# Performance work log

Measured on AMD Instinct MI355X. Metric: run time of the kernel, lower is better.

Reference implementation:

```python
import jax, jax.numpy as jnp
import numpy as np

VOCAB, HID, EMB, KSZ, VSZ = 34, 512, 128, 128, 128
T, N, L = 1024, 128, 200


def setup_inputs() -> dict:
    key = jax.random.key(0)
    ks = jax.random.split(key, 20)
    s = 0.05
    emb = jax.random.normal(ks[0], (VOCAB, EMB), jnp.float32) * s
    emb = emb.at[0].set(0.0)  # padding_idx=0
    inp = {
        "key_proj": jax.random.normal(ks[1], (T, N, KSZ), jnp.float32),
        "values": jax.random.normal(ks[2], (T, N, VSZ), jnp.float32),
        "reduced_length": jax.random.randint(ks[3], (N,), 1, T + 1),
        "text": jax.random.randint(ks[4], (N, L), 1, VOCAB),
        "embedding": emb,
        "Wq": jax.random.normal(ks[5], (KSZ, EMB), jnp.float32) * s,
        "bq": jnp.zeros((KSZ,), jnp.float32),
        "W_ih1": jax.random.normal(ks[6], (4 * HID, EMB + VSZ), jnp.float32) * s,
        "W_hh1": jax.random.normal(ks[7], (4 * HID, HID), jnp.float32) * s,
        "b_ih1": jnp.zeros((4 * HID,), jnp.float32),
        "b_hh1": jnp.zeros((4 * HID,), jnp.float32),
        "W_ih2": jax.random.normal(ks[8], (4 * KSZ, HID), jnp.float32) * s,
        "W_hh2": jax.random.normal(ks[9], (4 * KSZ, KSZ), jnp.float32) * s,
        "b_ih2": jnp.zeros((4 * KSZ,), jnp.float32),
        "b_hh2": jnp.zeros((4 * KSZ,), jnp.float32),
        "Wfc": jax.random.normal(ks[10], (EMB, KSZ * 2), jnp.float32) * s,
        "bfc": jnp.zeros((EMB,), jnp.float32),
        "b_out": jnp.zeros((VOCAB,), jnp.float32),
    }
    return inp


def _lstm_cell(x, h, c, Wih, Whh, bih, bhh):
    g = x @ Wih.T + bih + h @ Whh.T + bhh
    i, f, gg, o = jnp.split(g, 4, axis=1)
    c = jax.nn.sigmoid(f) * c + jax.nn.sigmoid(i) * jnp.tanh(gg)
    h = jax.nn.sigmoid(o) * jnp.tanh(c)
    return h, c


def reference(key_proj, values, reduced_length, text, embedding, Wq, bq,
              W_ih1, W_hh1, b_ih1, b_hh1, W_ih2, W_hh2, b_ih2, b_hh2,
              Wfc, bfc, b_out):
    n, l = text.shape
    keyT = jnp.transpose(key_proj, (1, 0, 2))   # (N,T,K)
    valT = jnp.transpose(values, (1, 0, 2))     # (N,T,V)
    t_len = keyT.shape[1]
    mask = jnp.arange(t_len)[None, :] >= reduced_length[:, None]  # (N,T) True=pad

    def attend(q):  # q: (N,K)
        energy = jnp.einsum('ntk,nk->nt', keyT, q)
        energy = jnp.where(mask, -1e9, energy)
        att = jax.nn.softmax(energy, axis=1)
        ctx = jnp.einsum('nt,ntv->nv', att, valT)
        return ctx

    # deterministic teacher forcing: step 0 uses embedding[0] (padding row),
    # step i uses embedding of text[:, i-1]
    char_seq = jnp.concatenate(
        [jnp.broadcast_to(embedding[0], (n, 1, embedding.shape[1])),
         embedding[text[:, :-1]]], axis=1)          # (N,L,E)
    char_seq = jnp.transpose(char_seq, (1, 0, 2))   # (L,N,E)

    h1 = jnp.zeros((n, W_hh1.shape[1]), jnp.float32)
    c1 = jnp.zeros_like(h1)
    h2 = jnp.zeros((n, W_hh2.shape[1]), jnp.float32)
    c2 = jnp.zeros_like(h2)

    def step(carry, ce):
        h1, c1, h2, c2 = carry
        q1 = ce @ Wq.T + bq
        ctx1 = attend(q1)
        inp = jnp.concatenate([ce, ctx1], axis=1)
        h1, c1 = _lstm_cell(inp, h1, c1, W_ih1, W_hh1, b_ih1, b_hh1)
        h2, c2 = _lstm_cell(h1, h2, c2, W_ih2, W_hh2, b_ih2, b_hh2)
        q2 = h2 @ Wq.T + bq
        ctx2 = attend(q2)
        out = jnp.concatenate([h2, ctx2], axis=1) @ Wfc.T + bfc
        out = jnp.clip(out, -1.0, 1.0)  # Hardtanh
        pred = out @ embedding.T + b_out  # tied output weights
        return (h1, c1, h2, c2), pred

    _, preds = jax.lax.scan(step, (h1, c1, h2, c2), char_seq)  # (L,N,V)
    return jnp.transpose(preds, (1, 0, 2))  # (N,L,V)
```

## Files before the change

kernel.cpp:

```cpp
#include <hip/hip_runtime.h>
#include <hip/hip_bf16.h>
#include <math.h>

#define T_LEN 1024
#define NB    128
#define L_SEQ 200
#define EMB   128
#define KSZ   128
#define VSZ   128
#define HID   512
#define G1    2048
#define G2    512
#define VOCAB 34
#define KK1   768
#define KK2   640
#define LB    10

typedef __attribute__((ext_vector_type(8))) short bf16x8;
typedef __attribute__((ext_vector_type(4))) float f32x4;

__device__ __forceinline__ float sig_(float x) { return 1.0f / (1.0f + __expf(-x)); }

__device__ __forceinline__ f32x4 MFMA_BF16(bf16x8 a, bf16x8 b, f32x4 c) {
    return __builtin_amdgcn_mfma_f32_16x16x32_bf16(a, b, c, 0, 0, 0);
}
__device__ __forceinline__ bf16x8 LD8(const __hip_bfloat16* p) {
    return *(const bf16x8*)p;
}

__global__ __launch_bounds__(256) void prep_kernel(
    const float* __restrict__ Wih1, const float* __restrict__ Whh1,
    const float* __restrict__ bih1, const float* __restrict__ bhh1,
    const float* __restrict__ Wih2, const float* __restrict__ Whh2,
    const float* __restrict__ bih2, const float* __restrict__ bhh2,
    __hip_bfloat16* __restrict__ Wc1, __hip_bfloat16* __restrict__ Wc2,
    float* __restrict__ bb1, float* __restrict__ bb2,
    __hip_bfloat16* __restrict__ h1b, __hip_bfloat16* __restrict__ h2b,
    float* __restrict__ c1, float* __restrict__ c2)
{
    const int gid = blockIdx.x * 256 + threadIdx.x;
    if (gid < G1 * KK1) {
        const int o = gid / KK1, k = gid - o * KK1;
        const float v = (k < 256) ? Wih1[o * 256 + k] : Whh1[o * 512 + (k - 256)];
        Wc1[gid] = __float2bfloat16(v);
    }
    if (gid < G2 * KK2) {
        const int o = gid / KK2, k = gid - o * KK2;
        const float v = (k < 512) ? Wih2[o * 512 + k] : Whh2[o * 128 + (k - 512)];
        Wc2[gid] = __float2bfloat16(v);
    }
    if (gid < G1) bb1[gid] = bih1[gid] + bhh1[gid];
    if (gid < G2) bb2[gid] = bih2[gid] + bhh2[gid];
    if (gid < 2 * NB * HID) h1b[gid] = __float2bfloat16(0.0f);
    if (gid < 2 * NB * KSZ) h2b[gid] = __float2bfloat16(0.0f);
    if (gid < NB * HID) c1[gid] = 0.0f;
    if (gid < NB * KSZ) c2[gid] = 0.0f;
}

__global__ __launch_bounds__(256) void transpose_key(
    const float* __restrict__ key, float* __restrict__ keyT2)
{
    __shared__ float tl[32][129];
    const int n = blockIdx.x >> 5;
    const int t0 = (blockIdx.x & 31) << 5;
    for (int idx = threadIdx.x; idx < 32 * 128; idx += 256) {
        const int ti = idx >> 7, k = idx & 127;
        tl[ti][k] = key[((size_t)(t0 + ti) * NB + n) * KSZ + k];
    }
    __syncthreads();
    for (int idx = threadIdx.x; idx < 32 * 128; idx += 256) {
        const int k = idx >> 5, ti = idx & 31;
        keyT2[((size_t)n * KSZ + k) * T_LEN + t0 + ti] = tl[ti][k];
    }
}

__global__ __launch_bounds__(256) void ce_gather(
    const int* __restrict__ text, const float* __restrict__ emb,
    float* __restrict__ ce_f, __hip_bfloat16* __restrict__ ce_b)
{
    const int idx = blockIdx.x * 256 + threadIdx.x;
    const int k = idx & 127;
    const int rn = idx >> 7;
    const int nn = rn & 127;
    const int s = rn >> 7;
    if (s >= L_SEQ) return;
    const int tok = (s == 0) ? 0 : text[nn * L_SEQ + (s - 1)];
    const float v = emb[(size_t)tok * EMB + k];
    ce_f[idx] = v;
    ce_b[idx] = __float2bfloat16(v);
}

__global__ __launch_bounds__(256) void qproj_kernel(
    const float* __restrict__ src, const float* __restrict__ Wq,
    const float* __restrict__ bq, float* __restrict__ dst)
{
    __shared__ float xs[2][KSZ];
    const int tid = threadIdx.x;
    const int r0 = blockIdx.x * 2;
    xs[tid >> 7][tid & 127] = src[(size_t)(r0 + (tid >> 7)) * KSZ + (tid & 127)];
    __syncthreads();
    const int sub = tid >> 7, o = tid & 127;
    const float* wr = Wq + (size_t)o * KSZ;
    float acc = bq[o];
    #pragma unroll 8
    for (int k = 0; k < KSZ; k += 4) {
        const float4 w4 = *(const float4*)&wr[k];
        const float4 x4 = *(const float4*)&xs[sub][k];
        acc += w4.x * x4.x + w4.y * x4.y + w4.z * x4.z + w4.w * x4.w;
    }
    dst[(size_t)(r0 + sub) * KSZ + o] = acc;
}

__global__ __launch_bounds__(256) void attn_kernel(
    const float* __restrict__ q,
    const float* __restrict__ keyT2,
    const float* __restrict__ values,
    const int* __restrict__ rlen,
    float* __restrict__ ctx_f,
    __hip_bfloat16* __restrict__ ctx_b)
{
    __shared__ float q_s[LB][KSZ];
    __shared__ float e_s[LB][T_LEN];
    __shared__ float cpart[2][LB][VSZ];
    __shared__ float inv_s[LB];
    __shared__ float red[8];
    const int tid = threadIdx.x;
    const int n = blockIdx.x / 20;
    const int s0 = (blockIdx.x % 20) * LB;
    const int len = rlen[n];
    const int lenp = (len + 7) & ~7;

    for (int idx = tid; idx < LB * KSZ; idx += 256) {
        const int j = idx >> 7, k = idx & 127;
        q_s[j][k] = q[((size_t)(s0 + j) * NB + n) * KSZ + k];
    }
    __syncthreads();

    {
        const int nt = (len + 255) >> 8;
        float e[4][LB];
        #pragma unroll
        for (int ti = 0; ti < 4; ++ti)
            #pragma unroll
            for (int j = 0; j < LB; ++j) e[ti][j] = 0.0f;
        const float* kb = keyT2 + (size_t)n * KSZ * T_LEN + tid;
        for (int k = 0; k < KSZ; k += 4) {
            float4 q4[LB];
            #pragma unroll
            for (int j = 0; j < LB; ++j) q4[j] = *(const float4*)&q_s[j][k];
            #pragma unroll
            for (int ti = 0; ti < 4; ++ti) {
                if (ti < nt) {
                    const float* kp = kb + ti * 256;
                    const float k0 = kp[(size_t)(k + 0) * T_LEN];
                    const float k1 = kp[(size_t)(k + 1) * T_LEN];
                    const float k2 = kp[(size_t)(k + 2) * T_LEN];
                    const float k3 = kp[(size_t)(k + 3) * T_LEN];
                    #pragma unroll
                    for (int j = 0; j < LB; ++j)
                        e[ti][j] += k0 * q4[j].x + k1 * q4[j].y + k2 * q4[j].z + k3 * q4[j].w;
                }
            }
        }
        #pragma unroll
        for (int ti = 0; ti < 4; ++ti) {
            const int t = tid + ti * 256;
            if (t < len) {
                #pragma unroll
                for (int j = 0; j < LB; ++j) e_s[j][t] = e[ti][j];
            }
        }
    }
    __syncthreads();

    const int wid = tid >> 6, ln = tid & 63;
    for (int j = 0; j < LB; ++j) {
        float m = -3.0e38f;
        for (int t = tid; t < len; t += 256) m = fmaxf(m, e_s[j][t]);
        #pragma unroll
        for (int off = 32; off > 0; off >>= 1) m = fmaxf(m, __shfl_xor(m, off, 64));
        if (ln == 0) red[wid] = m;
        __syncthreads();
        m = fmaxf(fmaxf(red[0], red[1]), fmaxf(red[2], red[3]));
        float s = 0.0f;
        for (int t = tid; t < len; t += 256) {
            const float p = __expf(e_s[j][t] - m);
            e_s[j][t] = p;
            s += p;
        }
        for (int t = len + tid; t < lenp; t += 256) e_s[j][t] = 0.0f;
        #pragma unroll
        for (int off = 32; off > 0; off >>= 1) s += __shfl_xor(s, off, 64);
        if (ln == 0) red[4 + wid] = s;
        __syncthreads();
        if (tid == 0) inv_s[j] = 1.0f / (red[4] + red[5] + red[6] + red[7]);
        __syncthreads();
    }

    {
        const int half = tid >> 7;
        const int v = tid & 127;
        float acc[LB];
        #pragma unroll
        for (int j = 0; j < LB; ++j) acc[j] = 0.0f;
        for (int tq = 4 * half; tq < lenp; tq += 8) {
            const float* vp = values + ((size_t)tq * NB + n) * VSZ + v;
            const float v0 = vp[0];
            const float v1 = vp[(size_t)NB * VSZ];
            const float v2 = vp[(size_t)2 * NB * VSZ];
            const float v3 = vp[(size_t)3 * NB * VSZ];
            #pragma unroll
            for (int j = 0; j < LB; ++j) {
                const float4 p4 = *(const float4*)&e_s[j][tq];
                acc[j] += p4.x * v0 + p4.y * v1 + p4.z * v2 + p4.w * v3;
            }
        }
        #pragma unroll
        for (int j = 0; j < LB; ++j) cpart[half][j][v] = acc[j];
    }
    __syncthreads();
    for (int idx = tid; idx < LB * VSZ; idx += 256) {
        const int j = idx >> 7, v = idx & 127;
        const float r = (cpart[0][j][v] + cpart[1][j][v]) * inv_s[j];
        const size_t o = ((size_t)(s0 + j) * NB + n) * VSZ + v;
        ctx_f[o] = r;
        ctx_b[o] = __float2bfloat16(r);
    }
}

__global__ __launch_bounds__(256) void scan_phase(
    const int i,
    const __hip_bfloat16* __restrict__ Wc1, const __hip_bfloat16* __restrict__ Wc2,
    const float* __restrict__ bb1, const float* __restrict__ bb2,
    const __hip_bfloat16* __restrict__ ce_b, const __hip_bfloat16* __restrict__ ctx1_b,
    __hip_bfloat16* __restrict__ h1b, __hip_bfloat16* __restrict__ h2b,
    float* __restrict__ c1, float* __restrict__ c2,
    float* __restrict__ h2_all)
{
    const int tid = threadIdx.x;
    const int w = tid >> 6;
    const int lane = tid & 63;
    const int lrow = lane & 15;
    const int krow = (lane >> 4) * 8;
    const int rb = i & 1;
    const __hip_bfloat16* h1r = h1b + (size_t)rb * NB * HID;
    __hip_bfloat16* h1w = h1b + (size_t)(rb ^ 1) * NB * HID;
    const __hip_bfloat16* h2r = h2b + (size_t)rb * NB * KSZ;
    __hip_bfloat16* h2w = h2b + (size_t)(rb ^ 1) * NB * KSZ;
    __shared__ float gl[4][32][17];

    if (blockIdx.x < 32) {
        if (i == 0) return;
        const int s2 = i - 1;
        const int n0 = (blockIdx.x >> 3) * 32;
        const int og = blockIdx.x & 7;
        const int col = w * 128 + og * 16 + lrow;
        const __hip_bfloat16* brow = Wc2 + (size_t)col * KK2 + krow;
        const int n_a = n0 + lrow;
        const __hip_bfloat16* a0 = h1r + (size_t)n_a * HID + krow;
        const __hip_bfloat16* a1 = h1r + (size_t)(n_a + 16) * HID + krow;
        const __hip_bfloat16* g0 = h2r + (size_t)n_a * KSZ + krow;
        const __hip_bfloat16* g1 = h2r + (size_t)(n_a + 16) * KSZ + krow;
        f32x4 acc0 = {0.f, 0.f, 0.f, 0.f}, acc1 = {0.f, 0.f, 0.f, 0.f};
        #pragma unroll
        for (int kk = 0; kk < 16; ++kk) {
            const bf16x8 bf = LD8(brow + kk * 32);
            acc0 = MFMA_BF16(LD8(a0 + kk * 32), bf, acc0);
            acc1 = MFMA_BF16(LD8(a1 + kk * 32), bf, acc1);
        }
        #pragma unroll
        for (int kk = 0; kk < 4; ++kk) {
            const bf16x8 bf = LD8(brow + 512 + kk * 32);
            acc0 = MFMA_BF16(LD8(g0 + kk * 32), bf, acc0);
            acc1 = MFMA_BF16(LD8(g1 + kk * 32), bf, acc1);
        }
        const int rbase = (lane >> 4) * 4;
        #pragma unroll
        for (int r = 0; r < 4; ++r) {
            gl[w][rbase + r][lrow] = acc0[r];
            gl[w][16 + rbase + r][lrow] = acc1[r];
        }
        __syncthreads();
        #pragma unroll
        for (int it = 0; it < 2; ++it) {
            const int idx = tid + it * 256;
            const int nl = idx >> 4, oo = idx & 15;
            const int oc = og * 16 + oo;
            const float iv = gl[0][nl][oo] + bb2[oc];
            const float fv = gl[1][nl][oo] + bb2[128 + oc];
            const float gv = gl[2][nl][oo] + bb2[256 + oc];
            const float ov = gl[3][nl][oo] + bb2[384 + oc];
            const int nn = n0 + nl;
            const float cold = c2[nn * KSZ + oc];
            const float cn = sig_(fv) * cold + sig_(iv) * tanhf(gv);
            const float hn = sig_(ov) * tanhf(cn);
            c2[nn * KSZ + oc] = cn;
            h2w[nn * KSZ + oc] = __float2bfloat16(hn);
            h2_all[((size_t)s2 * NB + nn) * KSZ + oc] = hn;
        }
    } else {
        if (i >= L_SEQ) return;
        const int bid2 = blockIdx.x - 32;
        const int n0 = (bid2 >> 5) * 32;
        const int og = bid2 & 31;
        const int col = w * 512 + og * 16 + lrow;
        const __hip_bfloat16* brow = Wc1 + (size_t)col * KK1 + krow;
        const int n_a = n0 + lrow;
        const __hip_bfloat16* e0 = ce_b + ((size_t)i * NB + n_a) * EMB + krow;
        const __hip_bfloat16* e1 = ce_b + ((size_t)i * NB + n_a + 16) * EMB + krow;
        const __hip_bfloat16* x0 = ctx1_b + ((size_t)i * NB + n_a) * VSZ + krow;
        const __hip_bfloat16* x1 = ctx1_b + ((size_t)i * NB + n_a + 16) * VSZ + krow;
        const __hip_bfloat16* a0 = h1r + (size_t)n_a * HID + krow;
        const __hip_bfloat16* a1 = h1r + (size_t)(n_a + 16) * HID + krow;
        f32x4 acc0 = {0.f, 0.f, 0.f, 0.f}, acc1 = {0.f, 0.f, 0.f, 0.f};
        #pragma unroll
        for (int kk = 0; kk < 4; ++kk) {
            const bf16x8 bf = LD8(brow + kk * 32);
            acc0 = MFMA_BF16(LD8(e0 + kk * 32), bf, acc0);
            acc1 = MFMA_BF16(LD8(e1 + kk * 32), bf, acc1);
        }
        #pragma unroll
        for (int kk = 0; kk < 4; ++kk) {
            const bf16x8 bf = LD8(brow + 128 + kk * 32);
            acc0 = MFMA_BF16(LD8(x0 + kk * 32), bf, acc0);
            acc1 = MFMA_BF16(LD8(x1 + kk * 32), bf, acc1);
        }
        #pragma unroll
        for (int kk = 0; kk < 16; ++kk) {
            const bf16x8 bf = LD8(brow + 256 + kk * 32);
            acc0 = MFMA_BF16(LD8(a0 + kk * 32), bf, acc0);
            acc1 = MFMA_BF16(LD8(a1 + kk * 32), bf, acc1);
        }
        const int rbase = (lane >> 4) * 4;
        #pragma unroll
        for (int r = 0; r < 4; ++r) {
            gl[w][rbase + r][lrow] = acc0[r];
            gl[w][16 + rbase + r][lrow] = acc1[r];
        }
        __syncthreads();
        #pragma unroll
        for (int it = 0; it < 2; ++it) {
            const int idx = tid + it * 256;
            const int nl = idx >> 4, oo = idx & 15;
            const int oc = og * 16 + oo;
            const float iv = gl[0][nl][oo] + bb1[oc];
            const float fv = gl[1][nl][oo] + bb1[512 + oc];
            const float gv = gl[2][nl][oo] + bb1[1024 + oc];
            const float ov = gl[3][nl][oo] + bb1[1536 + oc];
            const int nn = n0 + nl;
            const float cold = c1[nn * HID + oc];
            const float cn = sig_(fv) * cold + sig_(iv) * tanhf(gv);
            const float hn = sig_(ov) * tanhf(cn);
            c1[nn * HID + oc] = cn;
            h1w[nn * HID + oc] = __float2bfloat16(hn);
        }
    }
}

__global__ __launch_bounds__(256) void outpred_kernel(
    const float* __restrict__ h2_all, const float* __restrict__ ctx2,
    const float* __restrict__ Wfc, const float* __restrict__ bfc,
    const float* __restrict__ emb, const float* __restrict__ b_out,
    float* __restrict__ out)
{
    __shared__ float xs[2][256];
    __shared__ float os[2][EMB];
    const int tid = threadIdx.x;
    const int r0 = blockIdx.x * 2;
    const int sub = tid >> 7, lane = tid & 127;
    const int r = r0 + sub;
    xs[sub][lane] = h2_all[(size_t)r * KSZ + lane];
    xs[sub][128 + lane] = ctx2[(size_t)r * VSZ + lane];
    __syncthreads();
    const float* wr = Wfc + (size_t)lane * 256;
    float acc = bfc[lane];
    #pragma unroll 8
    for (int k = 0; k < 256; k += 4) {
        const float4 w4 = *(const float4*)&wr[k];
        const float4 x4 = *(const float4*)&xs[sub][k];
        acc += w4.x * x4.x + w4.y * x4.y + w4.z * x4.z + w4.w * x4.w;
    }
    acc = fminf(1.0f, fmaxf(-1.0f, acc));
    os[sub][lane] = acc;
    __syncthreads();
    if (lane < VOCAB) {
        const float* er = emb + (size_t)lane * EMB;
        float a = b_out[lane];
        #pragma unroll 8
        for (int e = 0; e < EMB; e += 4) {
            const float4 e4 = *(const float4*)&er[e];
            const float4 x4 = *(const float4*)&os[sub][e];
            a += e4.x * x4.x + e4.y * x4.y + e4.z * x4.z + e4.w * x4.w;
        }
        const int s = r >> 7, nn = r & 127;
        out[((size_t)nn * L_SEQ + s) * VOCAB + lane] = a;
    }
}

extern "C" void kernel_launch(void* const* d_in, const int* in_sizes, int n_in,
                              void* d_out, int out_size, void* d_ws, size_t ws_size,
                              hipStream_t stream)
{
    (void)in_sizes; (void)n_in; (void)out_size; (void)ws_size;
    const float* key_proj = (const float*)d_in[0];
    const float* values   = (const float*)d_in[1];
    const int*   rlen     = (const int*)d_in[2];
    const int*   text     = (const int*)d_in[3];
    const float* emb      = (const float*)d_in[4];
    const float* Wq    = (const float*)d_in[5];
    const float* bq    = (const float*)d_in[6];
    const float* Wih1  = (const float*)d_in[7];
    const float* Whh1  = (const float*)d_in[8];
    const float* bih1  = (const float*)d_in[9];
    const float* bhh1  = (const float*)d_in[10];
    const float* Wih2  = (const float*)d_in[11];
    const float* Whh2  = (const float*)d_in[12];
    const float* bih2  = (const float*)d_in[13];
    const float* bhh2  = (const float*)d_in[14];
    const float* Wfc   = (const float*)d_in[15];
    const float* bfc   = (const float*)d_in[16];
    const float* b_out = (const float*)d_in[17];
    float* out = (float*)d_out;

    char* p = (char*)d_ws;
    auto take = [&p](size_t bytes) -> char* {
        char* r = p;
        p += (bytes + 255) & ~((size_t)255);
        return r;
    };
    float* keyT2 = (float*)take((size_t)NB * KSZ * T_LEN * 4);
    float* ce_f  = (float*)take((size_t)L_SEQ * NB * EMB * 4);
    __hip_bfloat16* ce_b  = (__hip_bfloat16*)take((size_t)L_SEQ * NB * EMB * 2);
    __hip_bfloat16* ctx_b = (__hip_bfloat16*)take((size_t)L_SEQ * NB * VSZ * 2);
    float* ctx_f  = (float*)take((size_t)L_SEQ * NB * VSZ * 4);
    float* qbuf   = (float*)take((size_t)L_SEQ * NB * KSZ * 4);
    float* h2_all = (float*)take((size_t)L_SEQ * NB * KSZ * 4);
    __hip_bfloat16* Wc1 = (__hip_bfloat16*)take((size_t)G1 * KK1 * 2);
    __hip_bfloat16* Wc2 = (__hip_bfloat16*)take((size_t)G2 * KK2 * 2);
    float* bb1 = (float*)take(G1 * 4);
    float* bb2 = (float*)take(G2 * 4);
    __hip_bfloat16* h1b = (__hip_bfloat16*)take((size_t)2 * NB * HID * 2);
    __hip_bfloat16* h2b = (__hip_bfloat16*)take((size_t)2 * NB * KSZ * 2);
    float* c1 = (float*)take((size_t)NB * HID * 4);
    float* c2 = (float*)take((size_t)NB * KSZ * 4);

    prep_kernel<<<6144, 256, 0, stream>>>(Wih1, Whh1, bih1, bhh1, Wih2, Whh2,
                                          bih2, bhh2, Wc1, Wc2, bb1, bb2,
                                          h1b, h2b, c1, c2);
    transpose_key<<<4096, 256, 0, stream>>>(key_proj, keyT2);
    ce_gather<<<12800, 256, 0, stream>>>(text, emb, ce_f, ce_b);
    qproj_kernel<<<12800, 256, 0, stream>>>(ce_f, Wq, bq, qbuf);
    attn_kernel<<<2560, 256, 0, stream>>>(qbuf, keyT2, values, rlen, ctx_f, ctx_b);
    for (int i = 0; i <= L_SEQ; ++i)
        scan_phase<<<160, 256, 0, stream>>>(i, Wc1, Wc2, bb1, bb2, ce_b, ctx_b,
                                            h1b, h2b, c1, c2, h2_all);
    qproj_kernel<<<12800, 256, 0, stream>>>(h2_all, Wq, bq, qbuf);
    attn_kernel<<<2560, 256, 0, stream>>>(qbuf, keyT2, values, rlen, ctx_f, ctx_b);
    outpred_kernel<<<12800, 256, 0, stream>>>(h2_all, ctx_f, Wfc, bfc, emb, b_out, out);
}
```

Measured before the change: 3.993 ms.

## Persistent scan kernel with group barriers and flash-style tiled attention

After: 5.875 ms. 1.47x slower.

```diff
diff --git a/kernel.cpp b/kernel.cpp
--- a/kernel.cpp
+++ b/kernel.cpp
@@ -14,18 +14,36 @@
 #define VOCAB 34
 #define KK1   768
 #define KK2   640
-#define LB    10
+#define TT    64
+#define NBLK  160
+#define GRP_BLKS 40
 
 typedef __attribute__((ext_vector_type(8))) short bf16x8;
 typedef __attribute__((ext_vector_type(4))) float f32x4;
 
 __device__ __forceinline__ float sig_(float x) { return 1.0f / (1.0f + __expf(-x)); }
+__device__ __forceinline__ float tanh_fast(float x) {
+    return 1.0f - 2.0f / (__expf(2.0f * x) + 1.0f);
+}
 
 __device__ __forceinline__ f32x4 MFMA_BF16(bf16x8 a, bf16x8 b, f32x4 c) {
     return __builtin_amdgcn_mfma_f32_16x16x32_bf16(a, b, c, 0, 0, 0);
 }
 __device__ __forceinline__ bf16x8 LD8(const __hip_bfloat16* p) {
     return *(const bf16x8*)p;
+}
+
+__device__ __forceinline__ void gbar_grp(int* bar, int tgt) {
+    __syncthreads();
+    if (threadIdx.x == 0) {
+        __hip_atomic_fetch_add(bar, 1, __ATOMIC_RELEASE, __HIP_MEMORY_SCOPE_AGENT);
+        const long long t0 = __builtin_amdgcn_s_memrealtime();
+        while (__hip_atomic_load(bar, __ATOMIC_ACQUIRE, __HIP_MEMORY_SCOPE_AGENT) < tgt) {
+            __builtin_amdgcn_s_sleep(8);
+            if (__builtin_amdgcn_s_memrealtime() - t0 > 2000000LL) break;
+        }
+    }
+    __syncthreads();
 }
 
 __global__ __launch_bounds__(256) void prep_kernel(
@@ -36,7 +54,7 @@
     __hip_bfloat16* __restrict__ Wc1, __hip_bfloat16* __restrict__ Wc2,
     float* __restrict__ bb1, float* __restrict__ bb2,
     __hip_bfloat16* __restrict__ h1b, __hip_bfloat16* __restrict__ h2b,
-    float* __restrict__ c1, float* __restrict__ c2)
+    float* __restrict__ c1, float* __restrict__ c2, int* __restrict__ bar)
 {
     const int gid = blockIdx.x * 256 + threadIdx.x;
     if (gid < G1 * KK1) {
@@ -55,23 +73,7 @@
     if (gid < 2 * NB * KSZ) h2b[gid] = __float2bfloat16(0.0f);
     if (gid < NB * HID) c1[gid] = 0.0f;
     if (gid < NB * KSZ) c2[gid] = 0.0f;
-}
-
-__global__ __launch_bounds__(256) void transpose_key(
-    const float* __restrict__ key, float* __restrict__ keyT2)
-{
-    __shared__ float tl[32][129];
-    const int n = blockIdx.x >> 5;
-    const int t0 = (blockIdx.x & 31) << 5;
-    for (int idx = threadIdx.x; idx < 32 * 128; idx += 256) {
-        const int ti = idx >> 7, k = idx & 127;
-        tl[ti][k] = key[((size_t)(t0 + ti) * NB + n) * KSZ + k];
-    }
-    __syncthreads();
-    for (int idx = threadIdx.x; idx < 32 * 128; idx += 256) {
-        const int k = idx >> 5, ti = idx & 31;
-        keyT2[((size_t)n * KSZ + k) * T_LEN + t0 + ti] = tl[ti][k];
-    }
+    if (gid < 256) bar[gid] = 0;
 }
 
 __global__ __launch_bounds__(256) void ce_gather(
@@ -113,246 +115,260 @@
 
 __global__ __launch_bounds__(256) void attn_kernel(
     const float* __restrict__ q,
-    const float* __restrict__ keyT2,
+    const float* __restrict__ key,
     const float* __restrict__ values,
     const int* __restrict__ rlen,
     float* __restrict__ ctx_f,
     __hip_bfloat16* __restrict__ ctx_b)
 {
-    __shared__ float q_s[LB][KSZ];
-    __shared__ float e_s[LB][T_LEN];
-    __shared__ float cpart[2][LB][VSZ];
-    __shared__ float inv_s[LB];
-    __shared__ float red[8];
+    __shared__ __align__(16) float q_s[52][128];
+    __shared__ __align__(16) float Kt[TT][129];
+    __shared__ __align__(16) float Vt[TT][129];
+    __shared__ __align__(16) float es[52][68];
+    __shared__ float mm[52], ss[52], al[52];
     const int tid = threadIdx.x;
-    const int n = blockIdx.x / 20;
-    const int s0 = (blockIdx.x % 20) * LB;
+    const int n = blockIdx.x >> 2;
+    const int l0 = (blockIdx.x & 3) * 50;
     const int len = rlen[n];
-    const int lenp = (len + 7) & ~7;
-
-    for (int idx = tid; idx < LB * KSZ; idx += 256) {
-        const int j = idx >> 7, k = idx & 127;
-        q_s[j][k] = q[((size_t)(s0 + j) * NB + n) * KSZ + k];
-    }
-    __syncthreads();
-
-    {
-        const int nt = (len + 255) >> 8;
-        float e[4][LB];
+
+    for (int idx = tid; idx < 52 * 128; idx += 256) {
+        const int l = idx >> 7, k = idx & 127;
+        q_s[l][k] = (l < 50) ? q[((size_t)(l0 + l) * NB + n) * KSZ + k] : 0.0f;
+    }
+    for (int l = tid; l < 52; l += 256) { mm[l] = -3.0e38f; ss[l] = 0.0f; }
+    float acc[25];
+    #pragma unroll
+    for (int j = 0; j < 25; ++j) acc[j] = 0.0f;
+    __syncthreads();
+
+    const int lg = tid >> 6, lane = tid & 63;
+    const int vv = tid & 127, hh = tid >> 7;
+    const int nt = (len + TT - 1) / TT;
+
+    for (int tt = 0; tt < nt; ++tt) {
+        const int tb = tt * TT;
+        const int valid = min(TT, len - tb);
         #pragma unroll
-        for (int ti = 0; ti < 4; ++ti)
+        for (int it = 0; it < 8; ++it) {
+            const int idx4 = tid + it * 256;
+            const int r = idx4 >> 5, c4 = (idx4 & 31) * 4;
+            float4 kq = make_float4(0.f, 0.f, 0.f, 0.f);
+            float4 vq = make_float4(0.f, 0.f, 0.f, 0.f);
+            if (r < valid) {
+                const size_t base = ((size_t)(tb + r) * NB + n) * 128 + c4;
+                kq = *(const float4*)&key[base];
+                vq = *(const float4*)&values[base];
+            }
+            Kt[r][c4 + 0] = kq.x; Kt[r][c4 + 1] = kq.y;
+            Kt[r][c4 + 2] = kq.z; Kt[r][c4 + 3] = kq.w;
+            Vt[r][c4 + 0] = vq.x; Vt[r][c4 + 1] = vq.y;
+            Vt[r][c4 + 2] = vq.z; Vt[r][c4 + 3] = vq.w;
+        }
+        __syncthreads();
+        {
+            float e[13];
             #pragma unroll
-            for (int j = 0; j < LB; ++j) e[ti][j] = 0.0f;
-        const float* kb = keyT2 + (size_t)n * KSZ * T_LEN + tid;
-        for (int k = 0; k < KSZ; k += 4) {
-            float4 q4[LB];
+            for (int j = 0; j < 13; ++j) e[j] = 0.0f;
+            for (int k4 = 0; k4 < 128; k4 += 4) {
+                const float c0 = Kt[lane][k4 + 0], c1 = Kt[lane][k4 + 1];
+                const float c2 = Kt[lane][k4 + 2], c3 = Kt[lane][k4 + 3];
+                #pragma unroll
+                for (int j = 0; j < 13; ++j) {
+                    const float4 q4 = *(const float4*)&q_s[lg * 13 + j][k4];
+                    e[j] += c0 * q4.x + c1 * q4.y + c2 * q4.z + c3 * q4.w;
+                }
+            }
             #pragma unroll
-            for (int j = 0; j < LB; ++j) q4[j] = *(const float4*)&q_s[j][k];
-            #pragma unroll
-            for (int ti = 0; ti < 4; ++ti) {
-                if (ti < nt) {
-                    const float* kp = kb + ti * 256;
-                    const float k0 = kp[(size_t)(k + 0) * T_LEN];
-                    const float k1 = kp[(size_t)(k + 1) * T_LEN];
-                    const float k2 = kp[(size_t)(k + 2) * T_LEN];
-                    const float k3 = kp[(size_t)(k + 3) * T_LEN];
-                    #pragma unroll
-                    for (int j = 0; j < LB; ++j)
-                        e[ti][j] += k0 * q4[j].x + k1 * q4[j].y + k2 * q4[j].z + k3 * q4[j].w;
-                }
-            }
-        }
+            for (int j = 0; j < 13; ++j) {
+                const int l = lg * 13 + j;
+                float ev = (lane < valid) ? e[j] : -3.0e38f;
+                #pragma unroll
+                for (int off = 32; off; off >>= 1) ev = fmaxf(ev, __shfl_xor(ev, off, 64));
+                const float mold = mm[l];
+                const float mnew = fmaxf(mold, ev);
+                const float p = (lane < valid) ? __expf(e[j] - mnew) : 0.0f;
+                es[l][lane] = p;
+                float ps = p;
+                #pragma unroll
+                for (int off = 32; off; off >>= 1) ps += __shfl_xor(ps, off, 64);
+                if (lane == 0) {
+                    const float a = __expf(mold - mnew);
+                    al[l] = a;
+                    ss[l] = ss[l] * a + ps;
+                    mm[l] = mnew;
+                }
+            }
+        }
+        __syncthreads();
         #pragma unroll
-        for (int ti = 0; ti < 4; ++ti) {
-            const int t = tid + ti * 256;
-            if (t < len) {
-                #pragma unroll
-                for (int j = 0; j < LB; ++j) e_s[j][t] = e[ti][j];
-            }
-        }
-    }
-    __syncthreads();
-
-    const int wid = tid >> 6, ln = tid & 63;
-    for (int j = 0; j < LB; ++j) {
-        float m = -3.0e38f;
-        for (int t = tid; t < len; t += 256) m = fmaxf(m, e_s[j][t]);
-        #pragma unroll
-        for (int off = 32; off > 0; off >>= 1) m = fmaxf(m, __shfl_xor(m, off, 64));
-        if (ln == 0) red[wid] = m;
+        for (int j = 0; j < 25; ++j) {
+            const int l = hh + 2 * j;
+            float a = acc[j] * al[l];
+            #pragma unroll 4
+            for (int t4 = 0; t4 < TT; t4 += 4) {
+                const float4 p4 = *(const float4*)&es[l][t4];
+                a += p4.x * Vt[t4 + 0][vv] + p4.y * Vt[t4 + 1][vv]
+                   + p4.z * Vt[t4 + 2][vv] + p4.w * Vt[t4 + 3][vv];
+            }
+            acc[j] = a;
+        }
         __syncthreads();
-        m = fmaxf(fmaxf(red[0], red[1]), fmaxf(red[2], red[3]));
-        float s = 0.0f;
-        for (int t = tid; t < len; t += 256) {
-            const float p = __expf(e_s[j][t] - m);
-            e_s[j][t] = p;
-            s += p;
-        }
-        for (int t = len + tid; t < lenp; t += 256) e_s[j][t] = 0.0f;
-        #pragma unroll
-        for (int off = 32; off > 0; off >>= 1) s += __shfl_xor(s, off, 64);
-        if (ln == 0) red[4 + wid] = s;
-        __syncthreads();
-        if (tid == 0) inv_s[j] = 1.0f / (red[4] + red[5] + red[6] + red[7]);
-        __syncthreads();
-    }
-
-    {
-        const int half = tid >> 7;
-        const int v = tid & 127;
-        float acc[LB];
-        #pragma unroll
-        for (int j = 0; j < LB; ++j) acc[j] = 0.0f;
-        for (int tq = 4 * half; tq < lenp; tq += 8) {
-            const float* vp = values + ((size_t)tq * NB + n) * VSZ + v;
-            const float v0 = vp[0];
-            const float v1 = vp[(size_t)NB * VSZ];
-            const float v2 = vp[(size_t)2 * NB * VSZ];
-            const float v3 = vp[(size_t)3 * NB * VSZ];
-            #pragma unroll
-            for (int j = 0; j < LB; ++j) {
-                const float4 p4 = *(const float4*)&e_s[j][tq];
-                acc[j] += p4.x * v0 + p4.y * v1 + p4.z * v2 + p4.w * v3;
-            }
-        }
-        #pragma unroll
-        for (int j = 0; j < LB; ++j) cpart[half][j][v] = acc[j];
-    }
-    __syncthreads();
-    for (int idx = tid; idx < LB * VSZ; idx += 256) {
-        const int j = idx >> 7, v = idx & 127;
-        const float r = (cpart[0][j][v] + cpart[1][j][v]) * inv_s[j];
-        const size_t o = ((size_t)(s0 + j) * NB + n) * VSZ + v;
+    }
+    #pragma unroll
+    for (int j = 0; j < 25; ++j) {
+        const int l = hh + 2 * j;
+        const float r = acc[j] / ss[l];
+        const size_t o = ((size_t)(l0 + l) * NB + n) * VSZ + vv;
         ctx_f[o] = r;
         ctx_b[o] = __float2bfloat16(r);
     }
 }
 
-__global__ __launch_bounds__(256) void scan_phase(
-    const int i,
+__global__ __launch_bounds__(256) void scan_persist(
     const __hip_bfloat16* __restrict__ Wc1, const __hip_bfloat16* __restrict__ Wc2,
     const float* __restrict__ bb1, const float* __restrict__ bb2,
     const __hip_bfloat16* __restrict__ ce_b, const __hip_bfloat16* __restrict__ ctx1_b,
     __hip_bfloat16* __restrict__ h1b, __hip_bfloat16* __restrict__ h2b,
     float* __restrict__ c1, float* __restrict__ c2,
-    float* __restrict__ h2_all)
+    float* __restrict__ h2_all, int* __restrict__ bar)
 {
     const int tid = threadIdx.x;
     const int w = tid >> 6;
     const int lane = tid & 63;
     const int lrow = lane & 15;
     const int krow = (lane >> 4) * 8;
-    const int rb = i & 1;
-    const __hip_bfloat16* h1r = h1b + (size_t)rb * NB * HID;
-    __hip_bfloat16* h1w = h1b + (size_t)(rb ^ 1) * NB * HID;
-    const __hip_bfloat16* h2r = h2b + (size_t)rb * NB * KSZ;
-    __hip_bfloat16* h2w = h2b + (size_t)(rb ^ 1) * NB * KSZ;
     __shared__ float gl[4][32][17];
 
     if (blockIdx.x < 32) {
-        if (i == 0) return;
-        const int s2 = i - 1;
-        const int n0 = (blockIdx.x >> 3) * 32;
+        const int grp = blockIdx.x >> 3;
+        int* gb = bar + grp * 64;
+        const int n0 = grp * 32;
         const int og = blockIdx.x & 7;
         const int col = w * 128 + og * 16 + lrow;
         const __hip_bfloat16* brow = Wc2 + (size_t)col * KK2 + krow;
-        const int n_a = n0 + lrow;
-        const __hip_bfloat16* a0 = h1r + (size_t)n_a * HID + krow;
-        const __hip_bfloat16* a1 = h1r + (size_t)(n_a + 16) * HID + krow;
-        const __hip_bfloat16* g0 = h2r + (size_t)n_a * KSZ + krow;
-        const __hip_bfloat16* g1 = h2r + (size_t)(n_a + 16) * KSZ + krow;
-        f32x4 acc0 = {0.f, 0.f, 0.f, 0.f}, acc1 = {0.f, 0.f, 0.f, 0.f};
+        bf16x8 wf[20];
         #pragma unroll
-        for (int kk = 0; kk < 16; ++kk) {
-            const bf16x8 bf = LD8(brow + kk * 32);
-            acc0 = MFMA_BF16(LD8(a0 + kk * 32), bf, acc0);
-            acc1 = MFMA_BF16(LD8(a1 + kk * 32), bf, acc1);
-        }
-        #pragma unroll
-        for (int kk = 0; kk < 4; ++kk) {
-            const bf16x8 bf = LD8(brow + 512 + kk * 32);
-            acc0 = MFMA_BF16(LD8(g0 + kk * 32), bf, acc0);
-            acc1 = MFMA_BF16(LD8(g1 + kk * 32), bf, acc1);
-        }
-        const int rbase = (lane >> 4) * 4;
-        #pragma unroll
-        for (int r = 0; r < 4; ++r) {
-            gl[w][rbase + r][lrow] = acc0[r];
-            gl[w][16 + rbase + r][lrow] = acc1[r];
-        }
-        __syncthreads();
-        #pragma unroll
-        for (int it = 0; it < 2; ++it) {
-            const int idx = tid + it * 256;
-            const int nl = idx >> 4, oo = idx & 15;
-            const int oc = og * 16 + oo;
-            const float iv = gl[0][nl][oo] + bb2[oc];
-            const float fv = gl[1][nl][oo] + bb2[128 + oc];
-            const float gv = gl[2][nl][oo] + bb2[256 + oc];
-            const float ov = gl[3][nl][oo] + bb2[384 + oc];
-            const int nn = n0 + nl;
-            const float cold = c2[nn * KSZ + oc];
-            const float cn = sig_(fv) * cold + sig_(iv) * tanhf(gv);
-            const float hn = sig_(ov) * tanhf(cn);
-            c2[nn * KSZ + oc] = cn;
-            h2w[nn * KSZ + oc] = __float2bfloat16(hn);
-            h2_all[((size_t)s2 * NB + nn) * KSZ + oc] = hn;
+        for (int kk = 0; kk < 20; ++kk) wf[kk] = LD8(brow + kk * 32);
+        const int oc_b = og * 16 + (tid & 15);
+        const float bi = bb2[oc_b],        bf_ = bb2[128 + oc_b];
+        const float bg = bb2[256 + oc_b],  bo  = bb2[384 + oc_b];
+        for (int i = 0; i <= L_SEQ; ++i) {
+            if (i >= 1) {
+                const int s2 = i - 1;
+                const int rb = i & 1;
+                const __hip_bfloat16* h1r = h1b + (size_t)rb * NB * HID;
+                const __hip_bfloat16* h2r = h2b + (size_t)rb * NB * KSZ;
+                __hip_bfloat16* h2w = h2b + (size_t)(rb ^ 1) * NB * KSZ;
+                const int n_a = n0 + lrow;
+                const __hip_bfloat16* a0 = h1r + (size_t)n_a * HID + krow;
+                const __hip_bfloat16* a1 = h1r + (size_t)(n_a + 16) * HID + krow;
+                const __hip_bfloat16* g0 = h2r + (size_t)n_a * KSZ + krow;
+                const __hip_bfloat16* g1 = h2r + (size_t)(n_a + 16) * KSZ + krow;
+                f32x4 acc0 = {0.f, 0.f, 0.f, 0.f}, acc1 = {0.f, 0.f, 0.f, 0.f};
+                #pragma unroll
+                for (int kk = 0; kk < 16; ++kk) {
+                    acc0 = MFMA_BF16(LD8(a0 + kk * 32), wf[kk], acc0);
+                    acc1 = MFMA_BF16(LD8(a1 + kk * 32), wf[kk], acc1);
+                }
+                #pragma unroll
+                for (int kk = 16; kk < 20; ++kk) {
+                    acc0 = MFMA_BF16(LD8(g0 + (kk - 16) * 32), wf[kk], acc0);
+                    acc1 = MFMA_BF16(LD8(g1 + (kk - 16) * 32), wf[kk], acc1);
+                }
+                const int rbase = (lane >> 4) * 4;
+                #pragma unroll
+                for (int r = 0; r < 4; ++r) {
+                    gl[w][rbase + r][lrow] = acc0[r];
+                    gl[w][16 + rbase + r][lrow] = acc1[r];
+                }
+                __syncthreads();
+                #pragma unroll
+                for (int it = 0; it < 2; ++it) {
+                    const int idx = tid + it * 256;
+                    const int nl = idx >> 4, oo = idx & 15;
+                    const int oc = og * 16 + oo;
+                    const float iv = gl[0][nl][oo] + bi;
+                    const float fv = gl[1][nl][oo] + bf_;
+                    const float gv = gl[2][nl][oo] + bg;
+                    const float ov = gl[3][nl][oo] + bo;
+                    const int nn = n0 + nl;
+                    const float cold = c2[nn * KSZ + oc];
+                    const float cn = sig_(fv) * cold + sig_(iv) * tanh_fast(gv);
+                    const float hn = sig_(ov) * tanh_fast(cn);
+                    c2[nn * KSZ + oc] = cn;
+                    h2w[nn * KSZ + oc] = __float2bfloat16(hn);
+                    h2_all[((size_t)s2 * NB + nn) * KSZ + oc] = hn;
+                }
+            }
+            if (i < L_SEQ) gbar_grp(gb, GRP_BLKS * (i + 1));
         }
     } else {
-        if (i >= L_SEQ) return;
         const int bid2 = blockIdx.x - 32;
-        const int n0 = (bid2 >> 5) * 32;
+        const int grp = bid2 >> 5;
+        int* gb = bar + grp * 64;
+        const int n0 = grp * 32;
         const int og = bid2 & 31;
         const int col = w * 512 + og * 16 + lrow;
         const __hip_bfloat16* brow = Wc1 + (size_t)col * KK1 + krow;
-        const int n_a = n0 + lrow;
-        const __hip_bfloat16* e0 = ce_b + ((size_t)i * NB + n_a) * EMB + krow;
-        const __hip_bfloat16* e1 = ce_b + ((size_t)i * NB + n_a + 16) * EMB + krow;
-        const __hip_bfloat16* x0 = ctx1_b + ((size_t)i * NB + n_a) * VSZ + krow;
-        const __hip_bfloat16* x1 = ctx1_b + ((size_t)i * NB + n_a + 16) * VSZ + krow;
-        const __hip_bfloat16* a0 = h1r + (size_t)n_a * HID + krow;
-        const __hip_bfloat16* a1 = h1r + (size_t)(n_a + 16) * HID + krow;
-        f32x4 acc0 = {0.f, 0.f, 0.f, 0.f}, acc1 = {0.f, 0.f, 0.f, 0.f};
+        bf16x8 wf[24];
         #pragma unroll
-        for (int kk = 0; kk < 4; ++kk) {
-            const bf16x8 bf = LD8(brow + kk * 32);
-            acc0 = MFMA_BF16(LD8(e0 + kk * 32), bf, acc0);
-            acc1 = MFMA_BF16(LD8(e1 + kk * 32), bf, acc1);
-        }
-        #pragma unroll
-        for (int kk = 0; kk < 4; ++kk) {
-            const bf16x8 bf = LD8(brow + 128 + kk * 32);
-            acc0 = MFMA_BF16(LD8(x0 + kk * 32), bf, acc0);
-            acc1 = MFMA_BF16(LD8(x1 + kk * 32), bf, acc1);
-        }
-        #pragma unroll
-        for (int kk = 0; kk < 16; ++kk) {
-            const bf16x8 bf = LD8(brow + 256 + kk * 32);
-            acc0 = MFMA_BF16(LD8(a0 + kk * 32), bf, acc0);
-            acc1 = MFMA_BF16(LD8(a1 + kk * 32), bf, acc1);
-        }
-        const int rbase = (lane >> 4) * 4;
-        #pragma unroll
-        for (int r = 0; r < 4; ++r) {
-            gl[w][rbase + r][lrow] = acc0[r];
-            gl[w][16 + rbase + r][lrow] = acc1[r];
-        }
-        __syncthreads();
-        #pragma unroll
-        for (int it = 0; it < 2; ++it) {
-            const int idx = tid + it * 256;
-            const int nl = idx >> 4, oo = idx & 15;
-            const int oc = og * 16 + oo;
-            const float iv = gl[0][nl][oo] + bb1[oc];
-            const float fv = gl[1][nl][oo] + bb1[512 + oc];
-            const float gv = gl[2][nl][oo] + bb1[1024 + oc];
-            const float ov = gl[3][nl][oo] + bb1[1536 + oc];
-            const int nn = n0 + nl;
-            const float cold = c1[nn * HID + oc];
-            const float cn = sig_(fv) * cold + sig_(iv) * tanhf(gv);
-            const float hn = sig_(ov) * tanhf(cn);
-            c1[nn * HID + oc] = cn;
-            h1w[nn * HID + oc] = __float2bfloat16(hn);
+        for (int kk = 0; kk < 24; ++kk) wf[kk] = LD8(brow + kk * 32);
+        const int oc_b = og * 16 + (tid & 15);
+        const float bi = bb1[oc_b],         bf_ = bb1[512 + oc_b];
+        const float bg = bb1[1024 + oc_b],  bo  = bb1[1536 + oc_b];
+        for (int i = 0; i <= L_SEQ; ++i) {
+            if (i < L_SEQ) {
+                const int rb = i & 1;
+                const __hip_bfloat16* h1r = h1b + (size_t)rb * NB * HID;
+                __hip_bfloat16* h1w = h1b + (size_t)(rb ^ 1) * NB * HID;
+                const int n_a = n0 + lrow;
+                const __hip_bfloat16* e0 = ce_b + ((size_t)i * NB + n_a) * EMB + krow;
+                const __hip_bfloat16* e1 = ce_b + ((size_t)i * NB + n_a + 16) * EMB + krow;
+                const __hip_bfloat16* x0 = ctx1_b + ((size_t)i * NB + n_a) * VSZ + krow;
+                const __hip_bfloat16* x1 = ctx1_b + ((size_t)i * NB + n_a + 16) * VSZ + krow;
+                const __hip_bfloat16* a0 = h1r + (size_t)n_a * HID + krow;
+                const __hip_bfloat16* a1 = h1r + (size_t)(n_a + 16) * HID + krow;
+                f32x4 acc0 = {0.f, 0.f, 0.f, 0.f}, acc1 = {0.f, 0.f, 0.f, 0.f};
+                #pragma unroll
+                for (int kk = 0; kk < 4; ++kk) {
+                    acc0 = MFMA_BF16(LD8(e0 + kk * 32), wf[kk], acc0);
+                    acc1 = MFMA_BF16(LD8(e1 + kk * 32), wf[kk], acc1);
+                }
+                #pragma unroll
+                for (int kk = 4; kk < 8; ++kk) {
+                    acc0 = MFMA_BF16(LD8(x0 + (kk - 4) * 32), wf[kk], acc0);
+                    acc1 = MFMA_BF16(LD8(x1 + (kk - 4) * 32), wf[kk], acc1);
+                }
+                #pragma unroll
+                for (int kk = 8; kk < 24; ++kk) {
+                    acc0 = MFMA_BF16(LD8(a0 + (kk - 8) * 32), wf[kk], acc0);
+                    acc1 = MFMA_BF16(LD8(a1 + (kk - 8) * 32), wf[kk], acc1);
+                }
+                const int rbase = (lane >> 4) * 4;
+                #pragma unroll
+                for (int r = 0; r < 4; ++r) {
+                    gl[w][rbase + r][lrow] = acc0[r];
+                    gl[w][16 + rbase + r][lrow] = acc1[r];
+                }
+                __syncthreads();
+                #pragma unroll
+                for (int it = 0; it < 2; ++it) {
+                    const int idx = tid + it * 256;
+                    const int nl = idx >> 4, oo = idx & 15;
+                    const int oc = og * 16 + oo;
+                    const float iv = gl[0][nl][oo] + bi;
+                    const float fv = gl[1][nl][oo] + bf_;
+                    const float gv = gl[2][nl][oo] + bg;
+                    const float ov = gl[3][nl][oo] + bo;
+                    const int nn = n0 + nl;
+                    const float cold = c1[nn * HID + oc];
+                    const float cn = sig_(fv) * cold + sig_(iv) * tanh_fast(gv);
+                    const float hn = sig_(ov) * tanh_fast(cn);
+                    c1[nn * HID + oc] = cn;
+                    h1w[nn * HID + oc] = __float2bfloat16(hn);
+                }
+            }
+            if (i < L_SEQ) gbar_grp(gb, GRP_BLKS * (i + 1));
         }
     }
 }
@@ -428,7 +444,6 @@
         p += (bytes + 255) & ~((size_t)255);
         return r;
     };
-    float* keyT2 = (float*)take((size_t)NB * KSZ * T_LEN * 4);
     float* ce_f  = (float*)take((size_t)L_SEQ * NB * EMB * 4);
     __hip_bfloat16* ce_b  = (__hip_bfloat16*)take((size_t)L_SEQ * NB * EMB * 2);
     __hip_bfloat16* ctx_b = (__hip_bfloat16*)take((size_t)L_SEQ * NB * VSZ * 2);
@@ -443,18 +458,17 @@
     __hip_bfloat16* h2b = (__hip_bfloat16*)take((size_t)2 * NB * KSZ * 2);
     float* c1 = (float*)take((size_t)NB * HID * 4);
     float* c2 = (float*)take((size_t)NB * KSZ * 4);
+    int* bar = (int*)take(1024);
 
     prep_kernel<<<6144, 256, 0, stream>>>(Wih1, Whh1, bih1, bhh1, Wih2, Whh2,
                                           bih2, bhh2, Wc1, Wc2, bb1, bb2,
-                                          h1b, h2b, c1, c2);
-    transpose_key<<<4096, 256, 0, stream>>>(key_proj, keyT2);
+                                          h1b, h2b, c1, c2, bar);
     ce_gather<<<12800, 256, 0, stream>>>(text, emb, ce_f, ce_b);
     qproj_kernel<<<12800, 256, 0, stream>>>(ce_f, Wq, bq, qbuf);
-    attn_kernel<<<2560, 256, 0, stream>>>(qbuf, keyT2, values, rlen, ctx_f, ctx_b);
-    for (int i = 0; i <= L_SEQ; ++i)
-        scan_phase<<<160, 256, 0, stream>>>(i, Wc1, Wc2, bb1, bb2, ce_b, ctx_b,
-                                            h1b, h2b, c1, c2, h2_all);
+    attn_kernel<<<512, 256, 0, stream>>>(qbuf, key_proj, values, rlen, ctx_f, ctx_b);
+    scan_persist<<<NBLK, 256, 0, stream>>>(Wc1, Wc2, bb1, bb2, ce_b, ctx_b,
+                                           h1b, h2b, c1, c2, h2_all, bar);
     qproj_kernel<<<12800, 256, 0, stream>>>(h2_all, Wq, bq, qbuf);
-    attn_kernel<<<2560, 256, 0, stream>>>(qbuf, keyT2, values, rlen, ctx_f, ctx_b);
+    attn_kernel<<<512, 256, 0, stream>>>(qbuf, key_proj, values, rlen, ctx_f, ctx_b);
     outpred_kernel<<<12800, 256, 0, stream>>>(h2_all, ctx_f, Wfc, bfc, emb, b_out, out);
 }
```
